# Kernel optimization log

Measured on AMD Instinct MI355X. Metric: run time of the kernel, lower is better.

The kernel has to match this reference:

```python
import jax, jax.numpy as jnp
import numpy as np

N_NODES = 32767   # complete binary tree, depth 15
EMB_DIM = 256
HIDDEN = 256      # 'hidden_size' -> LSTM state is 2*HIDDEN
VOCAB = 32        # len(ExprNode.TYPE_LIST)


def setup_inputs() -> dict:
    key = jax.random.key(0)
    k1, k2, k3, k4, k5, k6 = jax.random.split(key, 6)
    H2 = 2 * HIDDEN
    types = jax.random.randint(k1, (N_NODES,), 0, VOCAB, dtype=jnp.int32)
    # complete binary tree: children of node i are 2i+1 / 2i+2; sentinel slot N = zero state
    idx = np.arange(N_NODES)
    a = 2 * idx + 1
    b = 2 * idx + 2
    a = np.where(a < N_NODES, a, N_NODES).astype(np.int32)
    b = np.where(b < N_NODES, b, N_NODES).astype(np.int32)
    scale = 1.0 / np.sqrt(H2)
    return {
        "types": types,
        "a_idx": jnp.asarray(a),
        "b_idx": jnp.asarray(b),
        "emb": jax.random.normal(k2, (VOCAB, EMB_DIM), jnp.float32) * 0.02,
        "W_ih": jax.random.normal(k3, (4 * H2, EMB_DIM), jnp.float32) * scale,
        "W_hh": jax.random.normal(k4, (4 * H2, H2), jnp.float32) * scale,
        "b_ih": jax.random.normal(k5, (4 * H2,), jnp.float32) * scale,
        "b_hh": jax.random.normal(k6, (4 * H2,), jnp.float32) * scale,
    }


def reference(types, a_idx, b_idx, emb, W_ih, W_hh, b_ih, b_hh):
    """Recursive binary tree-LSTM over topological (leaves-first) order.
    Each node's LSTM state has size 2H; a parent's incoming (h, c) is the concat
    of the first H entries of each child's state (zeros for missing children).
    Returns per-node hidden outputs [N, 2H] (the out_map, indexed by node id)."""
    N = types.shape[0]
    H2 = W_hh.shape[1]
    H = H2 // 2
    # batched input projection for all nodes at once: [N, 4*H2]
    x_proj = emb[types] @ W_ih.T + (b_ih + b_hh)
    Hs0 = jnp.zeros((N + 1, H2), x_proj.dtype)  # slot N = h0 (zeros)
    Cs0 = jnp.zeros((N + 1, H2), x_proj.dtype)
    order = jnp.arange(N - 1, -1, -1)  # children (higher index) before parents

    def step(carry, i):
        Hs, Cs = carry
        h = jnp.concatenate([Hs[a_idx[i], :H], Hs[b_idx[i], :H]])  # [2H]
        c = jnp.concatenate([Cs[a_idx[i], :H], Cs[b_idx[i], :H]])
        gates = x_proj[i] + W_hh @ h                 # [4*H2], torch gate order i,f,g,o
        ig, fg, gg, og = jnp.split(gates, 4)
        c_new = jax.nn.sigmoid(fg) * c + jax.nn.sigmoid(ig) * jnp.tanh(gg)
        h_new = jax.nn.sigmoid(og) * jnp.tanh(c_new)
        return (Hs.at[i].set(h_new), Cs.at[i].set(c_new)), h_new

    _, outs = jax.lax.scan(step, (Hs0, Cs0), order)
    return outs[::-1]  # reorder so row i is node i's output
```

## Files before the change

### kernel.cpp

```cpp
#include <hip/hip_runtime.h>
#include <hip/hip_bf16.h>


#define NNODES 32767

typedef __attribute__((ext_vector_type(8))) short bf16x8;
typedef __attribute__((ext_vector_type(4))) float f32x4;

typedef const __attribute__((address_space(1))) void* gptr_t;
typedef __attribute__((address_space(3))) void* lptr_t;

__device__ __forceinline__ float sigf(float x) { return 1.0f / (1.0f + __expf(-x)); }
__device__ __forceinline__ float tanhfast(float x) { return 2.0f / (1.0f + __expf(-2.0f * x)) - 1.0f; }

__device__ __forceinline__ short bf_hi(float x) {
    __hip_bfloat16 h = __float2bfloat16(x);
    return __builtin_bit_cast(short, h);
}
__device__ __forceinline__ float bf_f(short s) {
    __hip_bfloat16 h = __builtin_bit_cast(__hip_bfloat16, s);
    return __bfloat162float(h);
}
__device__ __forceinline__ void split8(const float* src, short* hi, short* lo) {
#pragma unroll
    for (int j = 0; j < 8; ++j) {
        float x = src[j];
        short h = bf_hi(x);
        hi[j] = h;
        lo[j] = bf_hi(x - bf_f(h));
    }
}

__global__ void proj_kernel(const float* __restrict__ emb, const float* __restrict__ W_ih,
                            const float* __restrict__ b_ih, const float* __restrict__ b_hh,
                            float* __restrict__ proj) {
    __shared__ float e[256];
    int v = blockIdx.x >> 3;
    int rc = blockIdx.x & 7;
    int t = threadIdx.x;
    e[t] = emb[v * 256 + t];
    __syncthreads();
    int r = rc * 256 + t;
    const float4* w4 = (const float4*)(W_ih + (size_t)r * 256);
    const float4* e4 = (const float4*)e;
    float acc = 0.f;
#pragma unroll 8
    for (int k = 0; k < 64; ++k) {
        float4 w = w4[k];
        float4 h = e4[k];
        acc += w.x * h.x + w.y * h.y + w.z * h.z + w.w * h.w;
    }
    proj[v * 2048 + r] = acc + b_ih[r] + b_hh[r];
}

__global__ void wpack_kernel(const float* __restrict__ W_hh,
                             short* __restrict__ Whi, short* __restrict__ Wlo) {
    int t = blockIdx.x * 256 + threadIdx.x;
    int lane = t & 63;
    int kt = (t >> 6) & 15;
    int ntile = t >> 10;
    int n = ntile * 16 + (lane & 15);
    int k0 = kt * 32 + (lane >> 4) * 8;
    const float* src = W_hh + (size_t)n * 512 + k0;
    short hi[8], lo[8];
    split8(src, hi, lo);
    *(bf16x8*)(Whi + (size_t)t * 8) = *(bf16x8*)hi;
    *(bf16x8*)(Wlo + (size_t)t * 8) = *(bf16x8*)lo;
}

__global__ void leaf_kernel(const int* __restrict__ types, const float* __restrict__ proj,
                            float* __restrict__ out, float* __restrict__ C256,
                            short* __restrict__ Hsplit) {
    int bi = blockIdx.x;
    int node = 16383 + (bi >> 1);
    int j = ((bi & 1) << 8) + threadIdx.x;
    int tt = types[node];
    const float* p = proj + (size_t)tt * 2048;
    float gi = p[j];
    float gg = p[1024 + j];
    float go = p[1536 + j];
    float cn = sigf(gi) * tanhfast(gg);
    float hn = sigf(go) * tanhfast(cn);
    out[(size_t)node * 512 + j] = hn;
    if ((bi & 1) == 0) {
        C256[(size_t)node * 256 + j] = cn;
        short hi = bf_hi(hn);
        Hsplit[(size_t)node * 512 + j] = hi;
        Hsplit[(size_t)node * 512 + 256 + j] = bf_hi(hn - bf_f(hi));
    }
}

__global__ __launch_bounds__(512) void huge_gemm_lstm_kernel(
    const int* __restrict__ a_idx, const int* __restrict__ b_idx,
    const int* __restrict__ types, float* __restrict__ out,
    const float* __restrict__ proj, float* __restrict__ C256,
    short* __restrict__ Hsplit, int node_base) {
    __shared__ __align__(16) short lds[2][32768];
    __shared__ int sA[256], sB[256], sT[256];

    const unsigned WOFF = 16777216u;

    int t = threadIdx.x;
    int lin = blockIdx.x;
    int x = lin >> 3;
    int y = lin & 7;
    int node0 = node_base + x * 256;
    int j0 = y * 64;

    if (t < 256) {
        sA[t] = a_idx[node0 + t];
        sB[t] = b_idx[node0 + t];
        sT[t] = types[node0 + t];
    }
    __syncthreads();

    int w = t >> 6, lane = t & 63;
    int wm = w >> 2, wn = w & 3;

    unsigned b0[8], b1[8], sk;
    if (w < 4) {
        sk = 32u;
#pragma unroll
        for (int i = 0; i < 8; ++i) {
            int c = w * 8 + i;
            int mt = c >> 1, part = c & 1;
            int m_loc = mt * 16 + (lane & 15);
            unsigned ks = (unsigned)part * 256u + (unsigned)(lane >> 4) * 8u;
            b0[i] = (unsigned)sA[m_loc] * 512u + ks;
            b1[i] = (unsigned)sB[m_loc] * 512u + ks;
        }
    } else {
        sk = 512u;
#pragma unroll
        for (int i = 0; i < 8; ++i) {
            int cc = (w - 4) * 8 + i;
            int ntl = cc >> 1, part = cc & 1;
            int q = ntl >> 2, sub = ntl & 3;
            unsigned ntg = (unsigned)(q * 32 + y * 4 + sub);
            b0[i] = WOFF + ntg * 8192u + (unsigned)part * 1048576u + (unsigned)lane * 8u;
            b1[i] = b0[i] + 4096u;
        }
    }

    f32x4 acc[8][4];
#pragma unroll
    for (int i = 0; i < 8; ++i)
#pragma unroll
        for (int q = 0; q < 4; ++q) acc[i][q] = (f32x4){0.f, 0.f, 0.f, 0.f};

    auto stage = [&](int kt, int buf) {
#pragma unroll
        for (int i = 0; i < 8; ++i) {
            unsigned off = ((kt < 8) ? b0[i] : b1[i]) + (unsigned)(kt & 7) * sk;
            const short* gsrc = Hsplit + off;
            short* ldst = &lds[buf][(w * 8 + i) * 512];
            __builtin_amdgcn_global_load_lds((gptr_t)gsrc, (lptr_t)ldst, 16, 0, 0);
        }
    };

    auto compute = [&](int buf) {
        const short* L = lds[buf];
        bf16x8 bh[4], bl[4];
#pragma unroll
        for (int q = 0; q < 4; ++q) {
            int ci = 32 + (q * 4 + wn) * 2;
            bh[q] = *(const bf16x8*)&L[ci * 512 + lane * 8];
            bl[q] = *(const bf16x8*)&L[(ci + 1) * 512 + lane * 8];
        }
        __builtin_amdgcn_s_setprio(1);
#pragma unroll
        for (int i = 0; i < 8; ++i) {
            int mt = wm * 8 + i;
            bf16x8 ah = *(const bf16x8*)&L[(mt * 2) * 512 + lane * 8];
            bf16x8 al = *(const bf16x8*)&L[(mt * 2 + 1) * 512 + lane * 8];
#pragma unroll
            for (int q = 0; q < 4; ++q) {
                acc[i][q] = __builtin_amdgcn_mfma_f32_16x16x32_bf16(ah, bh[q], acc[i][q], 0, 0, 0);
                acc[i][q] = __builtin_amdgcn_mfma_f32_16x16x32_bf16(ah, bl[q], acc[i][q], 0, 0, 0);
                acc[i][q] = __builtin_amdgcn_mfma_f32_16x16x32_bf16(al, bh[q], acc[i][q], 0, 0, 0);
            }
        }
        __builtin_amdgcn_s_setprio(0);
    };

    stage(0, 0);
    int cur = 0;
#pragma unroll 1
    for (int kt = 0; kt < 16; ++kt) {
        __builtin_amdgcn_s_barrier();
        if (kt < 15) stage(kt + 1, cur ^ 1);
        if (kt < 15) {
            asm volatile("s_waitcnt vmcnt(8)" ::: "memory");
        } else {
            asm volatile("s_waitcnt vmcnt(0)" ::: "memory");
        }
        __builtin_amdgcn_s_barrier();
        compute(cur);
        cur ^= 1;
    }

    int j = j0 + wn * 16 + (lane & 15);
    bool fh = (j < 256);
    int jc = j & 255;
#pragma unroll
    for (int i = 0; i < 8; ++i) {
        int mrow = wm * 128 + i * 16 + (lane >> 4) * 4;
#pragma unroll
        for (int r = 0; r < 4; ++r) {
            int m_loc = mrow + r;
            int node = node0 + m_loc;
            const float* p = proj + (size_t)sT[m_loc] * 2048 + j;
            float gi = acc[i][0][r] + p[0];
            float gf = acc[i][1][r] + p[512];
            float gg = acc[i][2][r] + p[1024];
            float go = acc[i][3][r] + p[1536];
            int child = fh ? sA[m_loc] : sB[m_loc];
            float c = C256[(size_t)child * 256 + jc];
            float cn = sigf(gf) * c + sigf(gi) * tanhfast(gg);
            float hn = sigf(go) * tanhfast(cn);
            out[(size_t)node * 512 + j] = hn;
            if (fh) {
                C256[(size_t)node * 256 + j] = cn;
                short hi = bf_hi(hn);
                Hsplit[(size_t)node * 512 + j] = hi;
                Hsplit[(size_t)node * 512 + 256 + j] = bf_hi(hn - bf_f(hi));
            }
        }
    }
}

__global__ __launch_bounds__(256) void big_gemm_lstm_kernel(
    const int* __restrict__ a_idx, const int* __restrict__ b_idx,
    const int* __restrict__ types, float* __restrict__ out,
    const short* __restrict__ Whi,
    const float* __restrict__ proj, float* __restrict__ C256,
    short* __restrict__ Hsplit, int node_base) {
    __shared__ __align__(16) short lds[2][16384];
    __shared__ int sA[128], sB[128], sT[128];

    int t = threadIdx.x;
    int lin = blockIdx.x;
    int x = lin >> 4;
    int y = (lin & 7) * 2 + ((lin >> 3) & 1);
    int node0 = node_base + x * 128;
    int j0 = y * 32;

    if (t < 128) {
        sA[t] = a_idx[node0 + t];
        sB[t] = b_idx[node0 + t];
        sT[t] = types[node0 + t];
    }
    __syncthreads();

    int w = t >> 6, lane = t & 63;
    int wm = w >> 1, wn = w & 1;

    unsigned b0[8], b1[8];
    const short* tbl;
    unsigned stepk;
    if (w < 2) {
        tbl = Hsplit;
        stepk = 32;
#pragma unroll
        for (int i = 0; i < 8; ++i) {
            int c = w * 8 + i;
            int mt = c >> 1, part = c & 1;
            int m_loc = mt * 16 + (lane & 15);
            unsigned ks = (unsigned)part * 256u + (unsigned)(lane >> 4) * 8u;
            b0[i] = (unsigned)sA[m_loc] * 512u + ks;
            b1[i] = (unsigned)sB[m_loc] * 512u + ks;
        }
    } else {
        tbl = Whi;
        stepk = 512;
#pragma unroll
        for (int i = 0; i < 8; ++i) {
            int cc = (w - 2) * 8 + i;
            int nt = cc >> 1, part = cc & 1;
            int q = nt >> 1, sub = nt & 1;
            unsigned ntg = (unsigned)(q * 32 + y * 2 + sub);
            b0[i] = ntg * 8192u + (unsigned)part * 1048576u + (unsigned)lane * 8u;
            b1[i] = b0[i] + 4096u;
        }
    }

    f32x4 acc[4][4];
#pragma unroll
    for (int i = 0; i < 4; ++i)
#pragma unroll
        for (int q = 0; q < 4; ++q) acc[i][q] = (f32x4){0.f, 0.f, 0.f, 0.f};

    auto stage = [&](int kt, int buf) {
#pragma unroll
        for (int i = 0; i < 8; ++i) {
            unsigned off = ((kt < 8) ? b0[i] : b1[i]) + (unsigned)(kt & 7) * stepk;
            const short* gsrc = tbl + off;
            short* ldst = &lds[buf][(w * 8 + i) * 512];
            __builtin_amdgcn_global_load_lds((gptr_t)gsrc, (lptr_t)ldst, 16, 0, 0);
        }
    };

    auto compute = [&](int buf) {
        const short* L = lds[buf];
        bf16x8 ah[4], al[4];
#pragma unroll
        for (int i = 0; i < 4; ++i) {
            int mt = wm * 4 + i;
            ah[i] = *(const bf16x8*)&L[(mt * 2) * 512 + lane * 8];
            al[i] = *(const bf16x8*)&L[(mt * 2 + 1) * 512 + lane * 8];
        }
#pragma unroll
        for (int q = 0; q < 4; ++q) {
            int nt = q * 2 + wn;
            bf16x8 bh = *(const bf16x8*)&L[(16 + nt * 2) * 512 + lane * 8];
            bf16x8 bl = *(const bf16x8*)&L[(17 + nt * 2) * 512 + lane * 8];
#pragma unroll
            for (int i = 0; i < 4; ++i) {
                acc[i][q] = __builtin_amdgcn_mfma_f32_16x16x32_bf16(ah[i], bh, acc[i][q], 0, 0, 0);
                acc[i][q] = __builtin_amdgcn_mfma_f32_16x16x32_bf16(ah[i], bl, acc[i][q], 0, 0, 0);
                acc[i][q] = __builtin_amdgcn_mfma_f32_16x16x32_bf16(al[i], bh, acc[i][q], 0, 0, 0);
            }
        }
    };

    stage(0, 0);
    __syncthreads();
    for (int kt = 0; kt < 16; ++kt) {
        int cur = kt & 1;
        if (kt < 15) stage(kt + 1, cur ^ 1);
        compute(cur);
        __syncthreads();
    }

    int j = j0 + wn * 16 + (lane & 15);
    bool fh = (j < 256);
    int jc = j & 255;
#pragma unroll
    for (int i = 0; i < 4; ++i) {
        int mrow = wm * 64 + i * 16 + (lane >> 4) * 4;
#pragma unroll
        for (int r = 0; r < 4; ++r) {
            int m_loc = mrow + r;
            int node = node0 + m_loc;
            const float* p = proj + (size_t)sT[m_loc] * 2048 + j;
            float gi = acc[i][0][r] + p[0];
            float gf = acc[i][1][r] + p[512];
            float gg = acc[i][2][r] + p[1024];
            float go = acc[i][3][r] + p[1536];
            int child = fh ? sA[m_loc] : sB[m_loc];
            float c = C256[(size_t)child * 256 + jc];
            float cn = sigf(gf) * c + sigf(gi) * tanhfast(gg);
            float hn = sigf(go) * tanhfast(cn);
            out[(size_t)node * 512 + j] = hn;
            if (fh) {
                C256[(size_t)node * 256 + j] = cn;
                short hi = bf_hi(hn);
                Hsplit[(size_t)node * 512 + j] = hi;
                Hsplit[(size_t)node * 512 + 256 + j] = bf_hi(hn - bf_f(hi));
            }
        }
    }
}

__global__ __launch_bounds__(256) void gemm_lstm_kernel(
    const int* __restrict__ a_idx, const int* __restrict__ b_idx,
    const int* __restrict__ types, float* __restrict__ out,
    const short* __restrict__ Whi, const short* __restrict__ Wlo,
    const float* __restrict__ proj, float* __restrict__ C256,
    short* __restrict__ Hsplit, int node_base, int Jc) {
    __shared__ short Ahi[2][16][64][8];
    __shared__ short Alo[2][16][64][8];
    __shared__ int sA[32], sB[32], sT[32];
    int t = threadIdx.x;
    int node0 = node_base + blockIdx.x * 32;
    if (t < 32) {
        sA[t] = a_idx[node0 + t];
        sB[t] = b_idx[node0 + t];
        sT[t] = types[node0 + t];
    }
    __syncthreads();

#pragma unroll
    for (int it = 0; it < 8; ++it) {
        int c = it * 256 + t;
        int mt = c >> 10;
        int kt = (c >> 6) & 15;
        int lane = c & 63;
        int m_loc = mt * 16 + (lane & 15);
        int k0 = kt * 32 + (lane >> 4) * 8;
        int child = (k0 < 256) ? sA[m_loc] : sB[m_loc];
        const short* src = Hsplit + (size_t)child * 512 + (k0 & 255);
        *(bf16x8*)&Ahi[mt][kt][lane][0] = *(const bf16x8*)src;
        *(bf16x8*)&Alo[mt][kt][lane][0] = *(const bf16x8*)(src + 256);
    }
    __syncthreads();

    int w = t >> 6;
    int lane = t & 63;
    int jsteps = Jc >> 4;
    int jbase = blockIdx.y * Jc;

    auto epilogue = [&](int j0, f32x4 (&acc)[4][2]) {
        int j = j0 + (lane & 15);
        int jc = j & 255;
        bool fh = (j < 256);
#pragma unroll
        for (int mt = 0; mt < 2; ++mt) {
            int mrow = mt * 16 + (lane >> 4) * 4;
#pragma unroll
            for (int r = 0; r < 4; ++r) {
                int m_loc = mrow + r;
                int node = node0 + m_loc;
                const float* p = proj + (size_t)sT[m_loc] * 2048 + j;
                float gi = acc[0][mt][r] + p[0];
                float gf = acc[1][mt][r] + p[512];
                float gg = acc[2][mt][r] + p[1024];
                float go = acc[3][mt][r] + p[1536];
                int child = fh ? sA[m_loc] : sB[m_loc];
                float c = C256[(size_t)child * 256 + jc];
                float cn = sigf(gf) * c + sigf(gi) * tanhfast(gg);
                float hn = sigf(go) * tanhfast(cn);
                out[(size_t)node * 512 + j] = hn;
                if (fh) {
                    C256[(size_t)node * 256 + j] = cn;
                    short hi = bf_hi(hn);
                    Hsplit[(size_t)node * 512 + j] = hi;
                    Hsplit[(size_t)node * 512 + 256 + j] = bf_hi(hn - bf_f(hi));
                }
            }
        }
    };

    if (jsteps >= 4) {
        for (int js = w; js < jsteps; js += 4) {
            int j0 = jbase + js * 16;
            f32x4 acc[4][2];
#pragma unroll
            for (int q = 0; q < 4; ++q)
#pragma unroll
                for (int mt = 0; mt < 2; ++mt) acc[q][mt] = (f32x4){0.f, 0.f, 0.f, 0.f};
            int nt0 = j0 >> 4;
#pragma unroll 4
            for (int kt = 0; kt < 16; ++kt) {
                bf16x8 ah0 = *(const bf16x8*)&Ahi[0][kt][lane][0];
                bf16x8 al0 = *(const bf16x8*)&Alo[0][kt][lane][0];
                bf16x8 ah1 = *(const bf16x8*)&Ahi[1][kt][lane][0];
                bf16x8 al1 = *(const bf16x8*)&Alo[1][kt][lane][0];
#pragma unroll
                for (int q = 0; q < 4; ++q) {
                    int ntile = q * 32 + nt0;
                    size_t off = ((size_t)(ntile * 16 + kt) * 64 + lane) * 8;
                    bf16x8 bh = *(const bf16x8*)(Whi + off);
                    bf16x8 bl = *(const bf16x8*)(Wlo + off);
                    acc[q][0] = __builtin_amdgcn_mfma_f32_16x16x32_bf16(ah0, bh, acc[q][0], 0, 0, 0);
                    acc[q][0] = __builtin_amdgcn_mfma_f32_16x16x32_bf16(ah0, bl, acc[q][0], 0, 0, 0);
                    acc[q][0] = __builtin_amdgcn_mfma_f32_16x16x32_bf16(al0, bh, acc[q][0], 0, 0, 0);
                    acc[q][1] = __builtin_amdgcn_mfma_f32_16x16x32_bf16(ah1, bh, acc[q][1], 0, 0, 0);
                    acc[q][1] = __builtin_amdgcn_mfma_f32_16x16x32_bf16(ah1, bl, acc[q][1], 0, 0, 0);
                    acc[q][1] = __builtin_amdgcn_mfma_f32_16x16x32_bf16(al1, bh, acc[q][1], 0, 0, 0);
                }
            }
            epilogue(j0, acc);
        }
    } else {
        int js = w & 1;
        int khalf = w >> 1;
        int j0 = jbase + js * 16;
        f32x4 acc[4][2];
#pragma unroll
        for (int q = 0; q < 4; ++q)
#pragma unroll
            for (int mt = 0; mt < 2; ++mt) acc[q][mt] = (f32x4){0.f, 0.f, 0.f, 0.f};
        int nt0 = j0 >> 4;
        int kt0 = khalf * 8;
#pragma unroll 4
        for (int kt = kt0; kt < kt0 + 8; ++kt) {
            bf16x8 ah0 = *(const bf16x8*)&Ahi[0][kt][lane][0];
            bf16x8 al0 = *(const bf16x8*)&Alo[0][kt][lane][0];
            bf16x8 ah1 = *(const bf16x8*)&Ahi[1][kt][lane][0];
            bf16x8 al1 = *(const bf16x8*)&Alo[1][kt][lane][0];
#pragma unroll
            for (int q = 0; q < 4; ++q) {
                int ntile = q * 32 + nt0;
                size_t off = ((size_t)(ntile * 16 + kt) * 64 + lane) * 8;
                bf16x8 bh = *(const bf16x8*)(Whi + off);
                bf16x8 bl = *(const bf16x8*)(Wlo + off);
                acc[q][0] = __builtin_amdgcn_mfma_f32_16x16x32_bf16(ah0, bh, acc[q][0], 0, 0, 0);
                acc[q][0] = __builtin_amdgcn_mfma_f32_16x16x32_bf16(ah0, bl, acc[q][0], 0, 0, 0);
                acc[q][0] = __builtin_amdgcn_mfma_f32_16x16x32_bf16(al0, bh, acc[q][0], 0, 0, 0);
                acc[q][1] = __builtin_amdgcn_mfma_f32_16x16x32_bf16(ah1, bh, acc[q][1], 0, 0, 0);
                acc[q][1] = __builtin_amdgcn_mfma_f32_16x16x32_bf16(ah1, bl, acc[q][1], 0, 0, 0);
                acc[q][1] = __builtin_amdgcn_mfma_f32_16x16x32_bf16(al1, bh, acc[q][1], 0, 0, 0);
            }
        }
        __syncthreads();
        float* xch = (float*)&Ahi[0][0][0][0];
        if (khalf == 1) {
#pragma unroll
            for (int q = 0; q < 4; ++q)
#pragma unroll
                for (int mt = 0; mt < 2; ++mt)
                    *(f32x4*)&xch[(((q * 2 + mt) * 128) + js * 64 + lane) * 4] = acc[q][mt];
        }
        __syncthreads();
        if (khalf == 0) {
#pragma unroll
            for (int q = 0; q < 4; ++q)
#pragma unroll
                for (int mt = 0; mt < 2; ++mt) {
                    f32x4 o = *(const f32x4*)&xch[(((q * 2 + mt) * 128) + js * 64 + lane) * 4];
                    acc[q][mt] += o;
                }
            epilogue(j0, acc);
        }
    }
}

__global__ void small_gemm_kernel(
    const int* __restrict__ a_idx, const int* __restrict__ b_idx,
    const float* __restrict__ out, const float* __restrict__ W_hh,
    float* __restrict__ part, int node_base) {
    __shared__ float hs[64];
    int t = threadIdx.x;
    int n = blockIdx.x;
    int node = node_base + n;
    int kbase = blockIdx.z * 64;
    if (t < 16) {
        int child = (kbase < 256) ? a_idx[node] : b_idx[node];
        float4 v = ((const float4*)(out + (size_t)child * 512 + (kbase & 255)))[t];
        ((float4*)hs)[t] = v;
    }
    __syncthreads();
    int r = blockIdx.y * 256 + t;
    const float4* w4 = (const float4*)(W_hh + (size_t)r * 512 + kbase);
    const float4* h4 = (const float4*)hs;
    float acc = 0.f;
#pragma unroll
    for (int k = 0; k < 16; ++k) {
        float4 wv = w4[k];
        float4 hv = h4[k];
        acc += wv.x * hv.x + wv.y * hv.y + wv.z * hv.z + wv.w * hv.w;
    }
    part[((size_t)blockIdx.z * gridDim.x + n) * 2048 + r] = acc;
}

__global__ void small_combine_kernel(
    const int* __restrict__ a_idx, const int* __restrict__ b_idx,
    const int* __restrict__ types, const float* __restrict__ part,
    const float* __restrict__ proj, float* __restrict__ C256,
    short* __restrict__ Hsplit, float* __restrict__ out, int node_base, int B) {
    int bi = blockIdx.x;
    int n = bi >> 1;
    int j = ((bi & 1) << 8) + threadIdx.x;
    int node = node_base + n;
    float g[4] = {0.f, 0.f, 0.f, 0.f};
    for (int z = 0; z < 8; ++z) {
        const float* p = part + ((size_t)z * B + n) * 2048;
#pragma unroll
        for (int q = 0; q < 4; ++q) g[q] += p[q * 512 + j];
    }
    const float* p = proj + (size_t)types[node] * 2048 + j;
    float gi = g[0] + p[0];
    float gf = g[1] + p[512];
    float gg = g[2] + p[1024];
    float go = g[3] + p[1536];
    int child = (j < 256) ? a_idx[node] : b_idx[node];
    float c = C256[(size_t)child * 256 + (j & 255)];
    float cn = sigf(gf) * c + sigf(gi) * tanhfast(gg);
    float hn = sigf(go) * tanhfast(cn);
    out[(size_t)node * 512 + j] = hn;
    if (j < 256) {
        C256[(size_t)node * 256 + j] = cn;
        short hi = bf_hi(hn);
        Hsplit[(size_t)node * 512 + j] = hi;
        Hsplit[(size_t)node * 512 + 256 + j] = bf_hi(hn - bf_f(hi));
    }
}

extern "C" void kernel_launch(void* const* d_in, const int* in_sizes, int n_in,
                              void* d_out, int out_size, void* d_ws, size_t ws_size,
                              hipStream_t stream) {
    const int* types = (const int*)d_in[0];
    const int* a_idx = (const int*)d_in[1];
    const int* b_idx = (const int*)d_in[2];
    const float* emb = (const float*)d_in[3];
    const float* W_ih = (const float*)d_in[4];
    const float* W_hh = (const float*)d_in[5];
    const float* b_ih = (const float*)d_in[6];
    const float* b_hh = (const float*)d_in[7];
    float* out = (float*)d_out;

    float* ws = (float*)d_ws;
    float* proj = ws;
    float* C256 = ws + 65536;
    short* Hsplit = (short*)(C256 + 8388352);
    short* Whi = Hsplit + 16777216;
    short* Wlo = Whi + 1048576;
    float* part = (float*)(Wlo + 1048576);

    proj_kernel<<<256, 256, 0, stream>>>(emb, W_ih, b_ih, b_hh, proj);
    wpack_kernel<<<512, 256, 0, stream>>>(W_hh, Whi, Wlo);
    leaf_kernel<<<32768, 256, 0, stream>>>(types, proj, out, C256, Hsplit);

    for (int d = 13; d >= 0; --d) {
        int base = (1 << d) - 1;
        int B = 1 << d;
        if (B >= 4096) {
            huge_gemm_lstm_kernel<<<(B / 256) * 8, 512, 0, stream>>>(
                a_idx, b_idx, types, out, proj, C256, Hsplit, base);
        } else if (B >= 1024) {
            int X = B / 128;
            big_gemm_lstm_kernel<<<X * 16, 256, 0, stream>>>(
                a_idx, b_idx, types, out, Whi, proj, C256, Hsplit, base);
        } else if (B >= 32) {
            int bx = B / 32;
            int J = 2;
            while (bx * J < 512 && J < 16) J <<= 1;
            gemm_lstm_kernel<<<dim3(bx, J), 256, 0, stream>>>(
                a_idx, b_idx, types, out, Whi, Wlo, proj, C256, Hsplit, base, 512 / J);
        } else {
            small_gemm_kernel<<<dim3(B, 8, 8), 256, 0, stream>>>(
                a_idx, b_idx, out, W_hh, part, base);
            small_combine_kernel<<<B * 2, 256, 0, stream>>>(
                a_idx, b_idx, types, part, proj, C256, Hsplit, out, base, B);
        }
    }
}
```

Baseline: 453.2 us.

## Fuse small-level gemm and combine into one kernel, shift level thresholds

Tree levels with fewer than 32 nodes now run a single fused kernel instead of a split-K gemm kernel plus a combine kernel. Each block handles one node and a 64-column slice, stages chunks of W_hh in shared memory, reduces partial sums in LDS and applies the LSTM cell directly. This removes one launch per level and the global partial-sum buffer. The dispatch thresholds also move so the huge and big gemm paths start at larger batch sizes, which sends more levels to the smaller kernels. The fused kernel has less parallelism per node and stages weights through LDS with several barriers, which adds serial work.

After: 520.1 us. 1.15x slower.

```diff
diff --git a/kernel.cpp b/kernel.cpp
--- a/kernel.cpp
+++ b/kernel.cpp
@@ -516,64 +516,82 @@
     }
 }
 
-__global__ void small_gemm_kernel(
+__global__ __launch_bounds__(256) void tiny_kernel(
     const int* __restrict__ a_idx, const int* __restrict__ b_idx,
-    const float* __restrict__ out, const float* __restrict__ W_hh,
-    float* __restrict__ part, int node_base) {
-    __shared__ float hs[64];
+    const int* __restrict__ types, const float* __restrict__ W_hh,
+    const float* __restrict__ proj, float* __restrict__ C256,
+    short* __restrict__ Hsplit, float* __restrict__ out, int node_base) {
+    __shared__ float hs[512];
+    __shared__ float Wc[32 * 512];
+    __shared__ float psum[32][9];
+    __shared__ float gall[256];
+
     int t = threadIdx.x;
-    int n = blockIdx.x;
-    int node = node_base + n;
-    int kbase = blockIdx.z * 64;
-    if (t < 16) {
-        int child = (kbase < 256) ? a_idx[node] : b_idx[node];
-        float4 v = ((const float4*)(out + (size_t)child * 512 + (kbase & 255)))[t];
-        ((float4*)hs)[t] = v;
+    int node = node_base + blockIdx.x;
+    int cs = blockIdx.y;
+    int na = a_idx[node], nb = b_idx[node];
+
+    if (t < 128) {
+        int k = t * 4;
+        const float* src = (k < 256) ? (out + (size_t)na * 512 + k)
+                                     : (out + (size_t)nb * 512 + (k - 256));
+        *(float4*)&hs[k] = *(const float4*)src;
     }
     __syncthreads();
-    int r = blockIdx.y * 256 + t;
-    const float4* w4 = (const float4*)(W_hh + (size_t)r * 512 + kbase);
-    const float4* h4 = (const float4*)hs;
-    float acc = 0.f;
-#pragma unroll
-    for (int k = 0; k < 16; ++k) {
-        float4 wv = w4[k];
-        float4 hv = h4[k];
-        acc += wv.x * hv.x + wv.y * hv.y + wv.z * hv.z + wv.w * hv.w;
-    }
-    part[((size_t)blockIdx.z * gridDim.x + n) * 2048 + r] = acc;
-}
-
-__global__ void small_combine_kernel(
-    const int* __restrict__ a_idx, const int* __restrict__ b_idx,
-    const int* __restrict__ types, const float* __restrict__ part,
-    const float* __restrict__ proj, float* __restrict__ C256,
-    short* __restrict__ Hsplit, float* __restrict__ out, int node_base, int B) {
-    int bi = blockIdx.x;
-    int n = bi >> 1;
-    int j = ((bi & 1) << 8) + threadIdx.x;
-    int node = node_base + n;
-    float g[4] = {0.f, 0.f, 0.f, 0.f};
-    for (int z = 0; z < 8; ++z) {
-        const float* p = part + ((size_t)z * B + n) * 2048;
-#pragma unroll
-        for (int q = 0; q < 4; ++q) g[q] += p[q * 512 + j];
-    }
-    const float* p = proj + (size_t)types[node] * 2048 + j;
-    float gi = g[0] + p[0];
-    float gf = g[1] + p[512];
-    float gg = g[2] + p[1024];
-    float go = g[3] + p[1536];
-    int child = (j < 256) ? a_idx[node] : b_idx[node];
-    float c = C256[(size_t)child * 256 + (j & 255)];
-    float cn = sigf(gf) * c + sigf(gi) * tanhfast(gg);
-    float hn = sigf(go) * tanhfast(cn);
-    out[(size_t)node * 512 + j] = hn;
-    if (j < 256) {
-        C256[(size_t)node * 256 + j] = cn;
-        short hi = bf_hi(hn);
-        Hsplit[(size_t)node * 512 + j] = hi;
-        Hsplit[(size_t)node * 512 + 256 + j] = bf_hi(hn - bf_f(hi));
+
+    for (int ch = 0; ch < 8; ++ch) {
+        for (int u = 0; u < 16; ++u) {
+            int i4 = u * 256 + t;
+            int r = i4 >> 7;
+            int k4 = i4 & 127;
+            int m = ch * 32 + r;
+            int g = m >> 6, c = m & 63;
+            const float* src = W_hh + ((size_t)(g * 512 + cs * 64 + c) * 512) + k4 * 4;
+            *(float4*)&Wc[r * 512 + k4 * 4] = *(const float4*)src;
+        }
+        __syncthreads();
+        {
+            int r = t >> 3, ks = t & 7;
+            const float4* w4 = (const float4*)&Wc[r * 512 + ks * 64];
+            const float4* h4 = (const float4*)&hs[ks * 64];
+            float acc = 0.f;
+#pragma unroll
+            for (int k = 0; k < 16; ++k) {
+                float4 wv = w4[k];
+                float4 hv = h4[k];
+                acc += wv.x * hv.x + wv.y * hv.y + wv.z * hv.z + wv.w * hv.w;
+            }
+            psum[r][ks] = acc;
+        }
+        __syncthreads();
+        if (t < 32) {
+            float s = psum[t][0];
+#pragma unroll
+            for (int ks = 1; ks < 8; ++ks) s += psum[t][ks];
+            gall[ch * 32 + t] = s;
+        }
+        __syncthreads();
+    }
+
+    if (t < 64) {
+        int c = t;
+        int j = cs * 64 + c;
+        const float* p = proj + (size_t)types[node] * 2048 + j;
+        float gi = gall[c] + p[0];
+        float gf = gall[64 + c] + p[512];
+        float gg = gall[128 + c] + p[1024];
+        float go = gall[192 + c] + p[1536];
+        int child = (j < 256) ? na : nb;
+        float cc = C256[(size_t)child * 256 + (j & 255)];
+        float cn = sigf(gf) * cc + sigf(gi) * tanhfast(gg);
+        float hn = sigf(go) * tanhfast(cn);
+        out[(size_t)node * 512 + j] = hn;
+        if (j < 256) {
+            C256[(size_t)node * 256 + j] = cn;
+            short hi = bf_hi(hn);
+            Hsplit[(size_t)node * 512 + j] = hi;
+            Hsplit[(size_t)node * 512 + 256 + j] = bf_hi(hn - bf_f(hi));
+        }
     }
 }
 
@@ -596,7 +614,6 @@
     short* Hsplit = (short*)(C256 + 8388352);
     short* Whi = Hsplit + 16777216;
     short* Wlo = Whi + 1048576;
-    float* part = (float*)(Wlo + 1048576);
 
     proj_kernel<<<256, 256, 0, stream>>>(emb, W_ih, b_ih, b_hh, proj);
     wpack_kernel<<<512, 256, 0, stream>>>(W_hh, Whi, Wlo);
@@ -605,10 +622,10 @@
     for (int d = 13; d >= 0; --d) {
         int base = (1 << d) - 1;
         int B = 1 << d;
-        if (B >= 4096) {
+        if (B >= 8192) {
             huge_gemm_lstm_kernel<<<(B / 256) * 8, 512, 0, stream>>>(
                 a_idx, b_idx, types, out, proj, C256, Hsplit, base);
-        } else if (B >= 1024) {
+        } else if (B >= 2048) {
             int X = B / 128;
             big_gemm_lstm_kernel<<<X * 16, 256, 0, stream>>>(
                 a_idx, b_idx, types, out, Whi, proj, C256, Hsplit, base);
@@ -619,10 +636,8 @@
             gemm_lstm_kernel<<<dim3(bx, J), 256, 0, stream>>>(
                 a_idx, b_idx, types, out, Whi, Wlo, proj, C256, Hsplit, base, 512 / J);
         } else {
-            small_gemm_kernel<<<dim3(B, 8, 8), 256, 0, stream>>>(
-                a_idx, b_idx, out, W_hh, part, base);
-            small_combine_kernel<<<B * 2, 256, 0, stream>>>(
-                a_idx, b_idx, types, part, proj, C256, Hsplit, out, base, B);
-        }
-    }
-}
+            tiny_kernel<<<dim3(B, 8), 256, 0, stream>>>(
+                a_idx, b_idx, types, W_hh, proj, C256, Hsplit, out, base);
+        }
+    }
+}
```
